# Kernel optimization log

Measured on AMD Instinct MI355X. Metric: run time of the kernel, lower is better.

Reference implementation:

```python
import jax, jax.numpy as jnp
import numpy as np

DIM = 2048
N_HEADS = 16
Q_RANK = 1536
KV_RANK = 512
D_NOPE = 128
D_ROPE = 64
D_V = 128
EPS = 1e-6
B, S = 2, 2048
ROPE_THETA = 10000.0


def rmsnorm(x, w, eps=EPS):
    return x * jax.lax.rsqrt(jnp.mean(x * x, axis=-1, keepdims=True) + eps) * w


def apply_rope(x):
    # x: [b, h, s, d] with d even; LLaMA-style interleaved pair rotation
    b, h, s, d = x.shape
    inv_freq = 1.0 / (ROPE_THETA ** (jnp.arange(0, d, 2, dtype=jnp.float32) / d))
    ang = jnp.arange(s, dtype=jnp.float32)[:, None] * inv_freq[None, :]  # [s, d/2]
    cos, sin = jnp.cos(ang), jnp.sin(ang)
    xr = x.reshape(b, h, s, d // 2, 2)
    x1, x2 = xr[..., 0], xr[..., 1]
    o1 = x1 * cos - x2 * sin
    o2 = x1 * sin + x2 * cos
    return jnp.stack([o1, o2], axis=-1).reshape(b, h, s, d)


def setup_inputs() -> dict:
    key = jax.random.key(0)
    ks = jax.random.split(key, 10)
    std = 0.02
    return {
        "x": jax.random.normal(ks[0], (B, S, DIM), dtype=jnp.float32),
        "wq_down": jax.random.normal(ks[1], (Q_RANK, DIM), dtype=jnp.float32) * std,
        "q_norm_w": jnp.ones((Q_RANK,), dtype=jnp.float32),
        "wq_up": jax.random.normal(ks[2], (N_HEADS * D_NOPE, Q_RANK), dtype=jnp.float32) * std,
        "wq_rope": jax.random.normal(ks[3], (N_HEADS * D_ROPE, Q_RANK), dtype=jnp.float32) * std,
        "wkv_down": jax.random.normal(ks[4], (KV_RANK, DIM), dtype=jnp.float32) * std,
        "kv_norm_w": jnp.ones((KV_RANK,), dtype=jnp.float32),
        "wkv_up": jax.random.normal(ks[5], (N_HEADS * (D_NOPE + D_V), KV_RANK), dtype=jnp.float32) * std,
        "wk_rope": jax.random.normal(ks[6], (D_ROPE, DIM), dtype=jnp.float32) * std,
        "wo": jax.random.normal(ks[7], (DIM, N_HEADS * D_V), dtype=jnp.float32) * std,
    }


def reference(x, wq_down, q_norm_w, wq_up, wq_rope, wkv_down, kv_norm_w, wkv_up, wk_rope, wo):
    bs, s, _ = x.shape
    # low-rank Q path
    q_c = rmsnorm(x @ wq_down.T, q_norm_w)                              # [b,s,qr]
    q_nope = (q_c @ wq_up.T).reshape(bs, s, N_HEADS, D_NOPE).transpose(0, 2, 1, 3)
    q_pe = (q_c @ wq_rope.T).reshape(bs, s, N_HEADS, D_ROPE).transpose(0, 2, 1, 3)
    # low-rank KV path
    kv_c = rmsnorm(x @ wkv_down.T, kv_norm_w)                           # [b,s,kvr]
    kv_up = (kv_c @ wkv_up.T).reshape(bs, s, N_HEADS, D_NOPE + D_V)
    k_nope = kv_up[..., :D_NOPE].transpose(0, 2, 1, 3)                  # [b,h,s,dn]
    v = kv_up[..., D_NOPE:].transpose(0, 2, 1, 3)                       # [b,h,s,dv]
    # shared rope key (1 head), broadcast across heads
    k_rope = (x @ wk_rope.T).reshape(bs, s, 1, D_ROPE).transpose(0, 2, 1, 3)  # [b,1,s,dr]
    q_pe = apply_rope(q_pe)
    k_rope = apply_rope(k_rope)
    q = jnp.concatenate([q_nope, q_pe], axis=-1)                        # [b,h,s,dn+dr]
    k = jnp.concatenate([k_nope, jnp.broadcast_to(k_rope, (bs, N_HEADS, s, D_ROPE))], axis=-1)
    scale = 1.0 / np.sqrt(D_NOPE + D_ROPE)
    scores = jnp.einsum('bhqd,bhkd->bhqk', q, k) * scale                # [b,h,s,s]
    causal = jnp.tril(jnp.ones((s, s), dtype=bool))
    scores = jnp.where(causal, scores, -jnp.inf)
    probs = jax.nn.softmax(scores, axis=-1)
    out = jnp.einsum('bhqk,bhkv->bhqv', probs, v)                       # [b,h,s,dv]
    out = out.transpose(0, 2, 1, 3).reshape(bs, s, N_HEADS * D_V)
    return out @ wo.T
```

## Files before the change

### kernel.cpp

```cpp
#include <hip/hip_runtime.h>
#include <stdint.h>

typedef _Float16 f16x8 __attribute__((ext_vector_type(8)));
typedef _Float16 f16x4 __attribute__((ext_vector_type(4)));
typedef float fx4 __attribute__((ext_vector_type(4)));

static constexpr int S_LEN = 2048;
static constexpr int BATCH = 2;
static constexpr int TOKENS = BATCH * S_LEN;
static constexpr int DIM = 2048;
static constexpr int NH = 16;
static constexpr int QR = 1536;
static constexpr int KVR = 512;
static constexpr int DN = 128;
static constexpr int DR = 64;
static constexpr int DV = 128;

__device__ __forceinline__ void async16(const _Float16* g, _Float16* lds_base_uniform) {
  __builtin_amdgcn_global_load_lds(
      (const __attribute__((address_space(1))) void*)g,
      (__attribute__((address_space(3))) void*)lds_base_uniform, 16, 0, 0);
}

__device__ __forceinline__ void bar() {
  asm volatile("" ::: "memory");
  __builtin_amdgcn_s_barrier();
  asm volatile("" ::: "memory");
}
#define VMWAIT(n) asm volatile("s_waitcnt vmcnt(" #n ")" ::: "memory")

#define ROR16(x, ctrl) \
  __uint_as_float(__builtin_amdgcn_update_dpp(__float_as_uint(x), __float_as_uint(x), \
                                              (ctrl), 0xF, 0xF, false))

__device__ __forceinline__ void sincos_rev(float ang, float* sn, float* cs) {
  float rev = ang * 0.15915494309189535f;
  rev -= floorf(rev);
  *sn = __builtin_amdgcn_sinf(rev);
  *cs = __builtin_amdgcn_cosf(rev);
}

struct CvtSegs {
  const float* src[8];
  _Float16* dst[8];
  const float* nw[8];
  int nmod[8];
  int n4[8];
  int cum[9];
};
__global__ __launch_bounds__(256) void cvt_all(CvtSegs s) {
  const int b = blockIdx.x;
  int seg = 0;
#pragma unroll
  for (int k = 0; k < 7; ++k) seg += (b >= s.cum[seg + 1]) ? 1 : 0;
  const int i = (b - s.cum[seg]) * 256 + threadIdx.x;
  if (i >= s.n4[seg]) return;
  fx4 v = *(const fx4*)(s.src[seg] + (size_t)i * 4);
  if (s.nw[seg]) {
    const int c0 = (int)(((size_t)i * 4) % (size_t)s.nmod[seg]);
    fx4 wv = *(const fx4*)(s.nw[seg] + c0);
    v[0] *= wv[0]; v[1] *= wv[1]; v[2] *= wv[2]; v[3] *= wv[3];
  }
  f16x4 o;
  o[0] = (_Float16)v[0]; o[1] = (_Float16)v[1];
  o[2] = (_Float16)v[2]; o[3] = (_Float16)v[3];
  *(f16x4*)(s.dst[seg] + (size_t)i * 4) = o;
}

__global__ __launch_bounds__(256) void rownorm(const _Float16* __restrict__ qc,
                                               const _Float16* __restrict__ kvc,
                                               float* __restrict__ rq,
                                               float* __restrict__ rkv) {
  const int idx = blockIdx.x * 4 + (threadIdx.x >> 6);
  const int lane = threadIdx.x & 63;
  const bool isq = idx < TOKENS;
  const int row = isq ? idx : idx - TOKENS;
  const int NC = isq ? QR : KVR;
  const f16x8* p = (const f16x8*)((isq ? qc : kvc) + (size_t)row * NC);
  float ss = 0.f;
  for (int c = lane; c < NC / 8; c += 64) {
    f16x8 v = p[c];
#pragma unroll
    for (int e = 0; e < 8; ++e) { const float x = (float)v[e]; ss += x * x; }
  }
#pragma unroll
  for (int d = 1; d < 64; d <<= 1) ss += __shfl_xor(ss, d);
  if (lane == 0) {
    const float rv = rsqrtf(ss / (float)NC + 1e-6f);
    if (isq) rq[row] = rv; else rkv[row] = rv;
  }
}

template <int MODE>
__global__ __launch_bounds__(256) void gemm_nt(const _Float16* __restrict__ A,
                                               const _Float16* __restrict__ W,
                                               void* __restrict__ C0v,
                                               void* __restrict__ C1v,
                                               void* __restrict__ C2v,
                                               int M, int N, int K) {
  __shared__ __attribute__((aligned(16))) _Float16 As[3][128 * 32];
  __shared__ __attribute__((aligned(16))) _Float16 Ws[3][128 * 32];
  const int tid = threadIdx.x;
  const int lane = tid & 63;
  const int wave = tid >> 6;
  const int wr = (wave >> 1) * 64;
  const int wc = (wave & 1) * 64;
  const int m16 = lane & 15;
  const int quad = lane >> 4;
  const int swz = (m16 >> 1) & 3;
  const int m0 = blockIdx.y * 128;
  const int n0 = blockIdx.x * 128;

  auto stage = [&](int buf, int k0) {
#pragma unroll
    for (int p = 0; p < 2; ++p) {
      const int cb = p * 256 + wave * 64;
      const int ch = cb + lane;
      const int r = ch >> 2;
      const int c8 = ((ch & 3) ^ ((r >> 1) & 3)) * 8;
      async16(A + (size_t)(m0 + r) * K + k0 + c8, &As[buf][cb * 8]);
      async16(W + (size_t)(n0 + r) * K + k0 + c8, &Ws[buf][cb * 8]);
    }
  };

  const fx4 fz = {0.f, 0.f, 0.f, 0.f};
  fx4 acc[4][4];
#pragma unroll
  for (int i = 0; i < 4; ++i)
#pragma unroll
    for (int j = 0; j < 4; ++j) acc[i][j] = fz;

  const int nkt = K >> 5;
  stage(0, 0);
  stage(1, 32);
  int cur = 0;
  for (int kt = 0; kt < nkt; ++kt) {
    if (kt + 1 < nkt) { VMWAIT(4); } else { VMWAIT(0); }
    bar();
    if (kt + 2 < nkt) {
      int b2 = cur + 2; if (b2 >= 3) b2 -= 3;
      stage(b2, (kt + 2) * 32);
    }
    const _Float16* as = As[cur];
    const _Float16* ws = Ws[cur];
    f16x8 af[4], wf[4];
#pragma unroll
    for (int i = 0; i < 4; ++i)
      af[i] = *(const f16x8*)(&as[((wr + i * 16 + m16) * 4 + (quad ^ swz)) * 8]);
#pragma unroll
    for (int j = 0; j < 4; ++j)
      wf[j] = *(const f16x8*)(&ws[((wc + j * 16 + m16) * 4 + (quad ^ swz)) * 8]);
#pragma unroll
    for (int i = 0; i < 4; ++i)
#pragma unroll
      for (int j = 0; j < 4; ++j)
        acc[i][j] = __builtin_amdgcn_mfma_f32_16x16x32_f16(af[i], wf[j], acc[i][j], 0, 0, 0);
    if (++cur == 3) cur = 0;
  }

#pragma unroll
  for (int j = 0; j < 4; ++j) {
    const int col = n0 + wc + j * 16 + m16;
    if (MODE == 5) {
      if (col < 2048) {
#pragma unroll
        for (int i = 0; i < 4; ++i)
#pragma unroll
          for (int r = 0; r < 4; ++r) {
            const size_t row = (size_t)(m0 + wr + i * 16 + quad * 4 + r);
            const _Float16 v = (_Float16)acc[i][j][r];
            if (col < 1536) ((_Float16*)C0v)[row * 1536 + col] = v;
            else            ((_Float16*)C1v)[row * 512 + col - 1536] = v;
          }
      } else if (col < 2112) {
        const int d = col - 2048;
        const int pidx = d >> 1;
        const bool odd = (d & 1);
        const float fr = exp2f(-(float)pidx * 0.4152410118609203f);
#pragma unroll
        for (int i = 0; i < 4; ++i)
#pragma unroll
          for (int r = 0; r < 4; ++r) {
            const size_t row = (size_t)(m0 + wr + i * 16 + quad * 4 + r);
            const int spos = (int)(row & (S_LEN - 1));
            float sn, cs;
            sincos_rev((float)spos * fr, &sn, &cs);
            const float own = acc[i][j][r];
            const float oth = __shfl_xor(own, 1);
            const float res = odd ? (oth * sn + own * cs) : (own * cs - oth * sn);
            ((_Float16*)C2v)[row * 64 + d] = (_Float16)res;
          }
      }
    } else {
      if (col < N) {
#pragma unroll
        for (int i = 0; i < 4; ++i)
#pragma unroll
          for (int r = 0; r < 4; ++r) {
            const size_t row = (size_t)(m0 + wr + i * 16 + quad * 4 + r);
            ((float*)C0v)[row * N + col] = acc[i][j][r];
          }
      }
    }
  }
}

template <int MODE>
__global__ __launch_bounds__(512, 2) void gemm256(
    const _Float16* __restrict__ Aq, const _Float16* __restrict__ Wq,
    const _Float16* __restrict__ Akv, const _Float16* __restrict__ Wkv,
    const float* __restrict__ rq, const float* __restrict__ rkv,
    void* __restrict__ C0, void* __restrict__ C1,
    void* __restrict__ C2, void* __restrict__ C3, int Kq) {
  __shared__ __attribute__((aligned(16))) _Float16 As[2][256 * 64];
  __shared__ __attribute__((aligned(16))) _Float16 Ws[2][256 * 64];

  const int tid = threadIdx.x;
  const int lane = tid & 63;
  const int wave = tid >> 6;
  const int wrow = wave >> 2;
  const int wcol = wave & 3;
  const int m16 = lane & 15;
  const int quad = lane >> 4;
  const int m0 = blockIdx.y * 256;

  const bool isq = (MODE == 0) || ((int)blockIdx.x < 12);
  const int n0 = (MODE == 0) ? blockIdx.x * 256
                             : (isq ? blockIdx.x * 256 : (blockIdx.x - 12) * 256);
  const _Float16* A = (MODE == 0) ? Aq : (isq ? Aq : Akv);
  const _Float16* W = (MODE == 0) ? Wq : (isq ? Wq : Wkv);
  const int K = (MODE == 0) ? Kq : (isq ? QR : KVR);

  auto stageHalf = [&](int buf, int k0, int tensor, int h) {
#pragma unroll
    for (int k = 0; k < 2; ++k) {
      const int cb = (wave * 2 + k) * 64;
      const int ch = cb + lane;
      const int r = ch >> 3;
      const int gc = (ch & 7) ^ (r & 7);
      const int grow = h * 128 + r;
      if (tensor == 0)
        async16(A + (size_t)(m0 + grow) * K + k0 + gc * 8,
                &As[buf][(h * 1024 + cb) * 8]);
      else
        async16(W + (size_t)(n0 + grow) * K + k0 + gc * 8,
                &Ws[buf][(h * 1024 + cb) * 8]);
    }
  };

  const fx4 fz = {0.f, 0.f, 0.f, 0.f};
  fx4 acc[8][4];
#pragma unroll
  for (int i = 0; i < 8; ++i)
#pragma unroll
    for (int j = 0; j < 4; ++j) acc[i][j] = fz;

  f16x8 af[4][2], wf0[2][2], wf1[2][2];

  auto rdA = [&](const _Float16* as, int mh) {
#pragma unroll
    for (int mg = 0; mg < 4; ++mg)
#pragma unroll
      for (int ks = 0; ks < 2; ++ks) {
        const int row = mh * 128 + mg * 32 + wrow * 16 + m16;
        af[mg][ks] = *(const f16x8*)(&as[(row * 8 + ((ks * 4 + quad) ^ (m16 & 7))) * 8]);
      }
  };
  auto rdB = [&](const _Float16* ws, int nh, f16x8 wf[2][2]) {
#pragma unroll
    for (int ng = 0; ng < 2; ++ng)
#pragma unroll
      for (int ks = 0; ks < 2; ++ks) {
        const int row = nh * 128 + ng * 64 + wcol * 16 + m16;
        wf[ng][ks] = *(const f16x8*)(&ws[(row * 8 + ((ks * 4 + quad) ^ (m16 & 7))) * 8]);
      }
  };
  auto quadMFMA = [&](int mh, int nh, f16x8 wf[2][2]) {
    __builtin_amdgcn_s_setprio(1);
#pragma unroll
    for (int ks = 0; ks < 2; ++ks)
#pragma unroll
      for (int mg = 0; mg < 4; ++mg)
#pragma unroll
        for (int ng = 0; ng < 2; ++ng)
          acc[mh * 4 + mg][nh * 2 + ng] = __builtin_amdgcn_mfma_f32_16x16x32_f16(
              af[mg][ks], wf[ng][ks], acc[mh * 4 + mg][nh * 2 + ng], 0, 0, 0);
    __builtin_amdgcn_s_setprio(0);
  };

  const int nkt = K >> 6;
  stageHalf(0, 0, 0, 0);
  stageHalf(0, 0, 1, 0);
  stageHalf(0, 0, 1, 1);
  stageHalf(0, 0, 0, 1);

  for (int t = 0; t < nkt; ++t) {
    const int cur = t & 1;
    const int nb = cur ^ 1;
    const int k0n = (t + 1) * 64;
    const bool more = (t + 1 < nkt);
    const _Float16* as = As[cur];
    const _Float16* ws = Ws[cur];

    VMWAIT(4);
    bar();
    rdA(as, 0);
    rdB(ws, 0, wf0);
    if (more) stageHalf(nb, k0n, 0, 0);
    quadMFMA(0, 0, wf0);

    if (more) { VMWAIT(4); } else { VMWAIT(2); }
    bar();
    rdB(ws, 1, wf1);
    if (more) stageHalf(nb, k0n, 1, 0);
    quadMFMA(0, 1, wf1);

    if (more) { VMWAIT(4); } else { VMWAIT(0); }
    bar();
    rdA(as, 1);
    if (more) stageHalf(nb, k0n, 1, 1);
    quadMFMA(1, 1, wf1);

    bar();
    if (more) stageHalf(nb, k0n, 0, 1);
    quadMFMA(1, 0, wf0);
  }

  float rsq[8][4];
  if (MODE == 1) {
    const float* rs = isq ? rq : rkv;
#pragma unroll
    for (int mg = 0; mg < 8; ++mg)
#pragma unroll
      for (int r = 0; r < 4; ++r)
        rsq[mg][r] = rs[m0 + mg * 32 + wrow * 16 + quad * 4 + r];
  }

#pragma unroll
  for (int ng = 0; ng < 4; ++ng) {
    const int col = n0 + ng * 64 + wcol * 16 + m16;
    if (MODE == 0) {
#pragma unroll
      for (int mg = 0; mg < 8; ++mg)
#pragma unroll
        for (int r = 0; r < 4; ++r) {
          const size_t row = (size_t)(m0 + mg * 32 + wrow * 16 + quad * 4 + r);
          ((float*)C0)[row * 2048 + col] = acc[mg][ng][r];
        }
    } else if (isq) {
#pragma unroll
      for (int mg = 0; mg < 8; ++mg)
#pragma unroll
        for (int r = 0; r < 4; ++r) {
          const size_t row = (size_t)(m0 + mg * 32 + wrow * 16 + quad * 4 + r);
          const _Float16 v = (_Float16)(acc[mg][ng][r] * rsq[mg][r]);
          if (col < 2048) ((_Float16*)C0)[row * 2048 + col] = v;
          else ((_Float16*)C1)[row * 1024 + col - 2048] = v;
        }
    } else {
      const int head = col >> 8;
      const int sub = col & 255;
      if (sub < 128) {
#pragma unroll
        for (int mg = 0; mg < 8; ++mg)
#pragma unroll
          for (int r = 0; r < 4; ++r) {
            const size_t row = (size_t)(m0 + mg * 32 + wrow * 16 + quad * 4 + r);
            ((_Float16*)C2)[row * 2048 + head * 128 + sub] =
                (_Float16)(acc[mg][ng][r] * rsq[mg][r]);
          }
      } else {
        const int dv = sub - 128;
#pragma unroll
        for (int mg = 0; mg < 8; ++mg) {
          f16x4 v;
#pragma unroll
          for (int r = 0; r < 4; ++r) v[r] = (_Float16)(acc[mg][ng][r] * rsq[mg][r]);
          *(f16x4*)(&((_Float16*)C3)[(size_t)(head * 128 + dv) * TOKENS + m0 +
                                     mg * 32 + wrow * 16 + quad * 4]) = v;
        }
      }
    }
  }
}

__global__ __launch_bounds__(512, 1) void gemm_out(
    const _Float16* __restrict__ A,
    const _Float16* __restrict__ W,
    float* __restrict__ C) {
  __shared__ __attribute__((aligned(16))) _Float16 As[2][128 * 64];
  __shared__ __attribute__((aligned(16))) _Float16 Ws[2][256 * 64];

  const int tid = threadIdx.x;
  const int lane = tid & 63;
  const int wave = tid >> 6;
  const int wrow = wave >> 2;
  const int wcol = wave & 3;
  const int m16 = lane & 15;
  const int quad = lane >> 4;
  const int m0 = blockIdx.y * 128;
  const int n0 = blockIdx.x * 256;
  const int K = NH * DV;

  auto stageA = [&](int buf, int k0) {
#pragma unroll
    for (int k = 0; k < 2; ++k) {
      const int cb = (wave * 2 + k) * 64;
      const int ch = cb + lane;
      const int r = ch >> 3;
      const int gc = (ch & 7) ^ (r & 7);
      async16(A + (size_t)(m0 + r) * K + k0 + gc * 8, &As[buf][cb * 8]);
    }
  };
  auto stageW = [&](int buf, int k0, int h) {
#pragma unroll
    for (int k = 0; k < 2; ++k) {
      const int cb = (wave * 2 + k) * 64;
      const int ch = cb + lane;
      const int r = ch >> 3;
      const int gc = (ch & 7) ^ (r & 7);
      async16(W + (size_t)(n0 + h * 128 + r) * K + k0 + gc * 8,
              &Ws[buf][(h * 1024 + cb) * 8]);
    }
  };

  const fx4 fz = {0.f, 0.f, 0.f, 0.f};
  fx4 acc[4][4];
#pragma unroll
  for (int i = 0; i < 4; ++i)
#pragma unroll
    for (int j = 0; j < 4; ++j) acc[i][j] = fz;

  f16x8 af[4][2], wf0[2][2], wf1[2][2];

  auto rdA = [&](const _Float16* as) {
#pragma unroll
    for (int mg = 0; mg < 4; ++mg)
#pragma unroll
      for (int ks = 0; ks < 2; ++ks) {
        const int row = mg * 32 + wrow * 16 + m16;
        af[mg][ks] = *(const f16x8*)(&as[(row * 8 + ((ks * 4 + quad) ^ (m16 & 7))) * 8]);
      }
  };
  auto rdB = [&](const _Float16* ws, int nh, f16x8 wf[2][2]) {
#pragma unroll
    for (int ng = 0; ng < 2; ++ng)
#pragma unroll
      for (int ks = 0; ks < 2; ++ks) {
        const int row = nh * 128 + ng * 64 + wcol * 16 + m16;
        wf[ng][ks] = *(const f16x8*)(&ws[(row * 8 + ((ks * 4 + quad) ^ (m16 & 7))) * 8]);
      }
  };
  auto halfMFMA = [&](int nh, f16x8 wf[2][2]) {
    __builtin_amdgcn_s_setprio(1);
#pragma unroll
    for (int ks = 0; ks < 2; ++ks)
#pragma unroll
      for (int mg = 0; mg < 4; ++mg)
#pragma unroll
        for (int ng = 0; ng < 2; ++ng)
          acc[mg][nh * 2 + ng] = __builtin_amdgcn_mfma_f32_16x16x32_f16(
              af[mg][ks], wf[ng][ks], acc[mg][nh * 2 + ng], 0, 0, 0);
    __builtin_amdgcn_s_setprio(0);
  };

  const int nkt = K >> 6;
  stageA(0, 0);
  stageW(0, 0, 0);
  stageW(0, 0, 1);

  for (int t = 0; t < nkt; ++t) {
    const int cur = t & 1;
    const int nb = cur ^ 1;
    const int k0n = (t + 1) * 64;
    const bool more = (t + 1 < nkt);
    const _Float16* as = As[cur];
    const _Float16* ws = Ws[cur];

    VMWAIT(2);
    bar();
    rdA(as);
    rdB(ws, 0, wf0);
    if (more) stageA(nb, k0n);
    halfMFMA(0, wf0);

    if (more) { VMWAIT(2); } else { VMWAIT(0); }
    bar();
    rdB(ws, 1, wf1);
    if (more) { stageW(nb, k0n, 0); stageW(nb, k0n, 1); }
    halfMFMA(1, wf1);
  }

#pragma unroll
  for (int ng = 0; ng < 4; ++ng) {
    const int col = n0 + ng * 64 + wcol * 16 + m16;
#pragma unroll
    for (int mg = 0; mg < 4; ++mg)
#pragma unroll
      for (int r = 0; r < 4; ++r) {
        const size_t row = (size_t)(m0 + mg * 32 + wrow * 16 + quad * 4 + r);
        C[row * 2048 + col] = acc[mg][ng][r];
      }
  }
}

__global__ __launch_bounds__(512, 2) void mla_attn(
    const _Float16* __restrict__ qn,
    const _Float16* __restrict__ qp,
    const _Float16* __restrict__ kn,
    const _Float16* __restrict__ kr,
    const _Float16* __restrict__ vT,
    _Float16* __restrict__ out)
{
  __shared__ __attribute__((aligned(16))) _Float16 Ks[2][768 * 8];
  __shared__ __attribute__((aligned(16))) _Float16 Vs[2][512 * 8];
  __shared__ __attribute__((aligned(16))) _Float16 Ps[8][16][40];

  const int bid = blockIdx.x;
  const int j = bid >> 5;
  const int bh = bid & 31;
  const int b = bh >> 4;
  const int h = bh & 15;
  const int q16 = 15 - j;
  const int qb = q16 * 128;
  const int tok0 = b * S_LEN;

  const int tid = threadIdx.x;
  const int lane = tid & 63;
  const int wave = tid >> 6;
  const int m16 = lane & 15;
  const int quad = lane >> 4;
  const int R0 = qb + wave * 16;

  auto stageKV = [&](int buf, int kbase) {
#pragma unroll
    for (int jj = 0; jj < 3; ++jj) {
      const int idx = wave * 3 + jj;
      if (idx < 12) {
        const int ch = idx * 2 + (lane >> 5);
        const int key = lane & 31;
        const _Float16* g = (ch < 16)
            ? kn + (size_t)(tok0 + kbase + key) * 2048 + h * 128 + ch * 8
            : kr + (size_t)(tok0 + kbase + key) * 64 + (ch - 16) * 8;
        async16(g, &Ks[buf][idx * 512]);
      } else if (idx < 20) {
        const int iv = idx - 12;
        const int p = iv * 64 + lane;
        const int L = p ^ ((p >> 3) & 3);
        const int dv = L >> 2;
        const int qcc = L & 3;
        async16(vT + (size_t)(h * 128 + dv) * TOKENS + tok0 + kbase + qcc * 8,
                &Vs[buf][iv * 512]);
      }
    }
  };

  const float scale2 = 0.07216878364870323f * 1.4426950408889634f;
  const fx4 fz = {0.f, 0.f, 0.f, 0.f};

  f16x8 qf[6];
  {
    const int srow = qb + wave * 16 + m16;
    const size_t t = (size_t)(tok0 + srow);
#pragma unroll
    for (int kk = 0; kk < 4; ++kk)
      qf[kk] = *(const f16x8*)(qn + t * 2048 + h * 128 + kk * 32 + quad * 8);
#pragma unroll
    for (int kk = 0; kk < 2; ++kk) {
      f16x8 v = *(const f16x8*)(qp + t * 1024 + h * 64 + kk * 32 + quad * 8);
      f16x8 o;
      const int i0 = kk * 16 + quad * 4;
#pragma unroll
      for (int jj = 0; jj < 4; ++jj) {
        const float ang = (float)srow * exp2f(-(float)(i0 + jj) * 0.4152410118609203f);
        float sn, cs;
        sincos_rev(ang, &sn, &cs);
        const float x1 = (float)v[2 * jj], x2 = (float)v[2 * jj + 1];
        o[2 * jj]     = (_Float16)(x1 * cs - x2 * sn);
        o[2 * jj + 1] = (_Float16)(x1 * sn + x2 * cs);
      }
      qf[4 + kk] = o;
    }
  }

  fx4 oacc[9];
#pragma unroll
  for (int n = 0; n < 9; ++n) oacc[n] = fz;
  float mst[4];
#pragma unroll
  for (int r = 0; r < 4; ++r) mst[r] = -3.0e38f;
  f16x8 vones;
#pragma unroll
  for (int e = 0; e < 8; ++e) vones[e] = (_Float16)1.0f;

  const int nkt = (qb >> 5) + 4;

  stageKV(0, 0);
  for (int kt = 0; kt < nkt; ++kt) {
    const int kbase = kt * 32;
    __syncthreads();
    if (kt + 1 < nkt) stageKV((kt + 1) & 1, kbase + 32);

    const bool live = (kbase <= R0 + 15);
    if (!live) continue;
    const _Float16* ks = Ks[kt & 1];
    const _Float16* vs = Vs[kt & 1];

    fx4 sc[2];
    sc[0] = fz; sc[1] = fz;
    __builtin_amdgcn_s_setprio(1);
#pragma unroll
    for (int kk = 0; kk < 6; ++kk) {
#pragma unroll
      for (int n = 0; n < 2; ++n) {
        f16x8 kf = *(const f16x8*)(&ks[(kk * 128 + quad * 32 + n * 16 + m16) * 8]);
        sc[n] = __builtin_amdgcn_mfma_f32_16x16x32_f16(qf[kk], kf, sc[n], 0, 0, 0);
      }
    }
    __builtin_amdgcn_s_setprio(0);

    f16x8 vf[8];
#pragma unroll
    for (int n8 = 0; n8 < 8; ++n8) {
      const int c0 = (n8 * 16 + m16) * 4 + quad;
      vf[n8] = *(const f16x8*)(&vs[(c0 ^ ((c0 >> 3) & 3)) * 8]);
    }

    const bool needmask = (kbase + 31 > R0);
    float alpha[4];
    bool any_upd = false;
#pragma unroll
    for (int r = 0; r < 4; ++r) {
      float v0 = sc[0][r] * scale2;
      float v1 = sc[1][r] * scale2;
      if (needmask) {
        const int qrow = R0 + quad * 4 + r;
        if (kbase + m16 > qrow)      v0 = -3.0e38f;
        if (kbase + 16 + m16 > qrow) v1 = -3.0e38f;
      }
      const float pre = fmaxf(v0, v1);
      float al = 1.0f;
      if (__any(pre > mst[r] + 10.0f)) {
        float mx = pre;
        mx = fmaxf(mx, ROR16(mx, 0x128));
        mx = fmaxf(mx, ROR16(mx, 0x124));
        mx = fmaxf(mx, ROR16(mx, 0x122));
        mx = fmaxf(mx, ROR16(mx, 0x121));
        const float mn = fmaxf(mst[r], mx);
        al = exp2f(mst[r] - mn);
        mst[r] = mn;
        any_upd = true;
      }
      alpha[r] = al;
      const float p0 = exp2f(v0 - mst[r]);
      const float p1 = exp2f(v1 - mst[r]);
      _Float16* pr = &Ps[wave][quad * 4 + r][0];
      pr[m16] = (_Float16)p0;
      pr[16 + m16] = (_Float16)p1;
    }
    if (any_upd) {
#pragma unroll
      for (int n8 = 0; n8 < 9; ++n8)
#pragma unroll
        for (int r = 0; r < 4; ++r) oacc[n8][r] *= alpha[r];
    }

    f16x8 pf = *(const f16x8*)(&Ps[wave][m16][quad * 8]);
    __builtin_amdgcn_s_setprio(1);
#pragma unroll
    for (int n8 = 0; n8 < 8; ++n8)
      oacc[n8] = __builtin_amdgcn_mfma_f32_16x16x32_f16(pf, vf[n8], oacc[n8], 0, 0, 0);
    oacc[8] = __builtin_amdgcn_mfma_f32_16x16x32_f16(pf, vones, oacc[8], 0, 0, 0);
    __builtin_amdgcn_s_setprio(0);
  }

  float inv[4];
#pragma unroll
  for (int r = 0; r < 4; ++r) inv[r] = 1.0f / oacc[8][r];
#pragma unroll
  for (int n8 = 0; n8 < 8; ++n8) {
#pragma unroll
    for (int r = 0; r < 4; ++r) {
      const size_t t = (size_t)(tok0 + qb + wave * 16 + quad * 4 + r);
      out[t * 2048 + h * 128 + n8 * 16 + m16] = (_Float16)(oacc[n8][r] * inv[r]);
    }
  }
}

extern "C" void kernel_launch(void* const* d_in, const int* in_sizes, int n_in,
                              void* d_out, int out_size, void* d_ws, size_t ws_size,
                              hipStream_t stream) {
  const float* x         = (const float*)d_in[0];
  const float* wq_down   = (const float*)d_in[1];
  const float* q_norm_w  = (const float*)d_in[2];
  const float* wq_up     = (const float*)d_in[3];
  const float* wq_rope   = (const float*)d_in[4];
  const float* wkv_down  = (const float*)d_in[5];
  const float* kv_norm_w = (const float*)d_in[6];
  const float* wkv_up    = (const float*)d_in[7];
  const float* wk_rope   = (const float*)d_in[8];
  const float* wo        = (const float*)d_in[9];
  float* out = (float*)d_out;

  char* ws = (char*)d_ws;
  size_t off = 0;
  auto alloc = [&](size_t bytes) {
    char* p = ws + off;
    off += (bytes + 255) & ~(size_t)255;
    return p;
  };
  _Float16* x_h     = (_Float16*)alloc((size_t)TOKENS * DIM * 2);
  _Float16* wA_h    = (_Float16*)alloc((size_t)2176 * DIM * 2);
  _Float16* wquqr_h = (_Float16*)alloc((size_t)3072 * QR * 2);
  _Float16* wkvu_h  = (_Float16*)alloc((size_t)NH * 256 * KVR * 2);
  _Float16* wo_h    = (_Float16*)alloc((size_t)DIM * NH * DV * 2);
  _Float16* qc_h    = (_Float16*)alloc((size_t)TOKENS * QR * 2);
  _Float16* kvc_h   = (_Float16*)alloc((size_t)TOKENS * KVR * 2);
  _Float16* qnope_h = (_Float16*)alloc((size_t)TOKENS * 2048 * 2);
  _Float16* qpe_h   = (_Float16*)alloc((size_t)TOKENS * 1024 * 2);
  _Float16* knope_h = (_Float16*)alloc((size_t)TOKENS * 2048 * 2);
  _Float16* vT_h    = (_Float16*)alloc((size_t)2048 * TOKENS * 2);
  _Float16* krope_h = (_Float16*)alloc((size_t)TOKENS * DR * 2);
  _Float16* attn_h  = (_Float16*)alloc((size_t)TOKENS * 2048 * 2);
  float* rq_h       = (float*)alloc((size_t)TOKENS * 4);
  float* rkv_h      = (float*)alloc((size_t)TOKENS * 4);

  CvtSegs cs;
  const float* srcs[8] = {x, wq_down, wq_up, wq_rope, wkv_down, wk_rope, wkv_up, wo};
  _Float16* dsts[8] = {x_h, wA_h, wquqr_h, wquqr_h + (size_t)2048 * QR,
                       wA_h + (size_t)1536 * DIM, wA_h + (size_t)2048 * DIM,
                       wkvu_h, wo_h};
  const float* nws[8] = {nullptr, nullptr, q_norm_w, q_norm_w, nullptr, nullptr,
                         kv_norm_w, nullptr};
  const int nmods[8] = {4, 4, QR, QR, 4, 4, KVR, 4};
  const size_t ns[8] = {(size_t)TOKENS * DIM, (size_t)QR * DIM, (size_t)2048 * QR,
                        (size_t)1024 * QR, (size_t)KVR * DIM, (size_t)DR * DIM,
                        (size_t)NH * 256 * KVR, (size_t)DIM * NH * DV};
  int cum = 0;
  for (int i = 0; i < 8; ++i) {
    cs.src[i] = srcs[i];
    cs.dst[i] = dsts[i];
    cs.nw[i] = nws[i];
    cs.nmod[i] = nmods[i];
    cs.n4[i] = (int)(ns[i] / 4);
    cs.cum[i] = cum;
    cum += (cs.n4[i] + 255) / 256;
  }
  cs.cum[8] = cum;
  cvt_all<<<dim3(cum), 256, 0, stream>>>(cs);

  const unsigned gm = TOKENS / 128;

  gemm_nt<5><<<dim3(17, gm), 256, 0, stream>>>(x_h, wA_h, qc_h, kvc_h, krope_h,
                                               TOKENS, 2112, DIM);
  rownorm<<<dim3(2 * TOKENS / 4), 256, 0, stream>>>(qc_h, kvc_h, rq_h, rkv_h);
  gemm256<1><<<dim3(12 + 16, TOKENS / 256), 512, 0, stream>>>(
      qc_h, wquqr_h, kvc_h, wkvu_h, rq_h, rkv_h,
      qnope_h, qpe_h, knope_h, vT_h, 0);
  mla_attn<<<dim3(512), 512, 0, stream>>>(qnope_h, qpe_h, knope_h, krope_h, vT_h, attn_h);
  gemm_out<<<dim3(8, 32), 512, 0, stream>>>(attn_h, wo_h, out);
}
```

Baseline: 440.3 us.

## Fuse RMSNorm statistics into a larger-tile down-projection GEMM epilogue

Replaces the 128x128 down-projection GEMM with a 512-thread 128x256-tile kernel that uses a double-buffered 64-wide K loop. Its epilogue also accumulates per-row sums of squares into global buffers with atomics. This removes the separate rownorm kernel and the re-read of qc/kvc it needed; the up-projection now computes rsqrt from those sums. The sum buffers are zeroed by an extra segment in the conversion kernel. Risks are a 288-block grid that slightly exceeds one wave of CUs, and padded weight rows that are computed but then discarded.

```diff
diff --git a/kernel.cpp b/kernel.cpp
--- a/kernel.cpp
+++ b/kernel.cpp
@@ -41,20 +41,27 @@
 }
 
 struct CvtSegs {
-  const float* src[8];
-  _Float16* dst[8];
-  const float* nw[8];
-  int nmod[8];
-  int n4[8];
-  int cum[9];
+  const float* src[9];
+  _Float16* dst[9];
+  const float* nw[9];
+  int nmod[9];
+  int n4[9];
+  int cum[10];
 };
 __global__ __launch_bounds__(256) void cvt_all(CvtSegs s) {
   const int b = blockIdx.x;
   int seg = 0;
 #pragma unroll
-  for (int k = 0; k < 7; ++k) seg += (b >= s.cum[seg + 1]) ? 1 : 0;
+  for (int k = 0; k < 8; ++k) seg += (b >= s.cum[seg + 1]) ? 1 : 0;
   const int i = (b - s.cum[seg]) * 256 + threadIdx.x;
   if (i >= s.n4[seg]) return;
+  if (!s.src[seg]) {
+    f16x4 z;
+    z[0] = (_Float16)0.f; z[1] = (_Float16)0.f;
+    z[2] = (_Float16)0.f; z[3] = (_Float16)0.f;
+    *(f16x4*)(s.dst[seg] + (size_t)i * 4) = z;
+    return;
+  }
   fx4 v = *(const fx4*)(s.src[seg] + (size_t)i * 4);
   if (s.nw[seg]) {
     const int c0 = (int)(((size_t)i * 4) % (size_t)s.nmod[seg]);
@@ -67,59 +74,45 @@
   *(f16x4*)(s.dst[seg] + (size_t)i * 4) = o;
 }
 
-__global__ __launch_bounds__(256) void rownorm(const _Float16* __restrict__ qc,
-                                               const _Float16* __restrict__ kvc,
-                                               float* __restrict__ rq,
-                                               float* __restrict__ rkv) {
-  const int idx = blockIdx.x * 4 + (threadIdx.x >> 6);
-  const int lane = threadIdx.x & 63;
-  const bool isq = idx < TOKENS;
-  const int row = isq ? idx : idx - TOKENS;
-  const int NC = isq ? QR : KVR;
-  const f16x8* p = (const f16x8*)((isq ? qc : kvc) + (size_t)row * NC);
-  float ss = 0.f;
-  for (int c = lane; c < NC / 8; c += 64) {
-    f16x8 v = p[c];
-#pragma unroll
-    for (int e = 0; e < 8; ++e) { const float x = (float)v[e]; ss += x * x; }
-  }
-#pragma unroll
-  for (int d = 1; d < 64; d <<= 1) ss += __shfl_xor(ss, d);
-  if (lane == 0) {
-    const float rv = rsqrtf(ss / (float)NC + 1e-6f);
-    if (isq) rq[row] = rv; else rkv[row] = rv;
-  }
-}
-
-template <int MODE>
-__global__ __launch_bounds__(256) void gemm_nt(const _Float16* __restrict__ A,
-                                               const _Float16* __restrict__ W,
-                                               void* __restrict__ C0v,
-                                               void* __restrict__ C1v,
-                                               void* __restrict__ C2v,
-                                               int M, int N, int K) {
-  __shared__ __attribute__((aligned(16))) _Float16 As[3][128 * 32];
-  __shared__ __attribute__((aligned(16))) _Float16 Ws[3][128 * 32];
+__global__ __launch_bounds__(512, 1) void gemm_down(
+    const _Float16* __restrict__ A,
+    const _Float16* __restrict__ W,
+    _Float16* __restrict__ qc, _Float16* __restrict__ kvc,
+    _Float16* __restrict__ kr,
+    float* __restrict__ sums_q, float* __restrict__ sums_kv) {
+  __shared__ __attribute__((aligned(16))) _Float16 As[2][128 * 64];
+  __shared__ __attribute__((aligned(16))) _Float16 Ws[2][256 * 64];
+
   const int tid = threadIdx.x;
   const int lane = tid & 63;
   const int wave = tid >> 6;
-  const int wr = (wave >> 1) * 64;
-  const int wc = (wave & 1) * 64;
+  const int wrow = wave >> 2;
+  const int wcol = wave & 3;
   const int m16 = lane & 15;
   const int quad = lane >> 4;
-  const int swz = (m16 >> 1) & 3;
   const int m0 = blockIdx.y * 128;
-  const int n0 = blockIdx.x * 128;
-
-  auto stage = [&](int buf, int k0) {
-#pragma unroll
-    for (int p = 0; p < 2; ++p) {
-      const int cb = p * 256 + wave * 64;
+  const int n0 = blockIdx.x * 256;
+  const int K = DIM;
+
+  auto stageA = [&](int buf, int k0) {
+#pragma unroll
+    for (int k = 0; k < 2; ++k) {
+      const int cb = (wave * 2 + k) * 64;
       const int ch = cb + lane;
-      const int r = ch >> 2;
-      const int c8 = ((ch & 3) ^ ((r >> 1) & 3)) * 8;
-      async16(A + (size_t)(m0 + r) * K + k0 + c8, &As[buf][cb * 8]);
-      async16(W + (size_t)(n0 + r) * K + k0 + c8, &Ws[buf][cb * 8]);
+      const int r = ch >> 3;
+      const int gc = (ch & 7) ^ (r & 7);
+      async16(A + (size_t)(m0 + r) * K + k0 + gc * 8, &As[buf][cb * 8]);
+    }
+  };
+  auto stageW = [&](int buf, int k0, int h) {
+#pragma unroll
+    for (int k = 0; k < 2; ++k) {
+      const int cb = (wave * 2 + k) * 64;
+      const int ch = cb + lane;
+      const int r = ch >> 3;
+      const int gc = (ch & 7) ^ (r & 7);
+      async16(W + (size_t)(n0 + h * 128 + r) * K + k0 + gc * 8,
+              &Ws[buf][(h * 1024 + cb) * 8]);
     }
   };
 
@@ -130,88 +123,134 @@
 #pragma unroll
     for (int j = 0; j < 4; ++j) acc[i][j] = fz;
 
-  const int nkt = K >> 5;
-  stage(0, 0);
-  stage(1, 32);
-  int cur = 0;
-  for (int kt = 0; kt < nkt; ++kt) {
-    if (kt + 1 < nkt) { VMWAIT(4); } else { VMWAIT(0); }
-    bar();
-    if (kt + 2 < nkt) {
-      int b2 = cur + 2; if (b2 >= 3) b2 -= 3;
-      stage(b2, (kt + 2) * 32);
-    }
+  f16x8 af[4][2], wf0[2][2], wf1[2][2];
+
+  auto rdA = [&](const _Float16* as) {
+#pragma unroll
+    for (int mg = 0; mg < 4; ++mg)
+#pragma unroll
+      for (int ks = 0; ks < 2; ++ks) {
+        const int row = mg * 32 + wrow * 16 + m16;
+        af[mg][ks] = *(const f16x8*)(&as[(row * 8 + ((ks * 4 + quad) ^ (m16 & 7))) * 8]);
+      }
+  };
+  auto rdB = [&](const _Float16* ws, int nh, f16x8 wf[2][2]) {
+#pragma unroll
+    for (int ng = 0; ng < 2; ++ng)
+#pragma unroll
+      for (int ks = 0; ks < 2; ++ks) {
+        const int row = nh * 128 + ng * 64 + wcol * 16 + m16;
+        wf[ng][ks] = *(const f16x8*)(&ws[(row * 8 + ((ks * 4 + quad) ^ (m16 & 7))) * 8]);
+      }
+  };
+  auto halfMFMA = [&](int nh, f16x8 wf[2][2]) {
+    __builtin_amdgcn_s_setprio(1);
+#pragma unroll
+    for (int ks = 0; ks < 2; ++ks)
+#pragma unroll
+      for (int mg = 0; mg < 4; ++mg)
+#pragma unroll
+        for (int ng = 0; ng < 2; ++ng)
+          acc[mg][nh * 2 + ng] = __builtin_amdgcn_mfma_f32_16x16x32_f16(
+              af[mg][ks], wf[ng][ks], acc[mg][nh * 2 + ng], 0, 0, 0);
+    __builtin_amdgcn_s_setprio(0);
+  };
+
+  const int nkt = K >> 6;
+  stageA(0, 0);
+  stageW(0, 0, 0);
+  stageW(0, 0, 1);
+
+  for (int t = 0; t < nkt; ++t) {
+    const int cur = t & 1;
+    const int nb = cur ^ 1;
+    const int k0n = (t + 1) * 64;
+    const bool more = (t + 1 < nkt);
     const _Float16* as = As[cur];
     const _Float16* ws = Ws[cur];
-    f16x8 af[4], wf[4];
-#pragma unroll
-    for (int i = 0; i < 4; ++i)
-      af[i] = *(const f16x8*)(&as[((wr + i * 16 + m16) * 4 + (quad ^ swz)) * 8]);
-#pragma unroll
-    for (int j = 0; j < 4; ++j)
-      wf[j] = *(const f16x8*)(&ws[((wc + j * 16 + m16) * 4 + (quad ^ swz)) * 8]);
-#pragma unroll
-    for (int i = 0; i < 4; ++i)
-#pragma unroll
-      for (int j = 0; j < 4; ++j)
-        acc[i][j] = __builtin_amdgcn_mfma_f32_16x16x32_f16(af[i], wf[j], acc[i][j], 0, 0, 0);
-    if (++cur == 3) cur = 0;
-  }
-
-#pragma unroll
-  for (int j = 0; j < 4; ++j) {
-    const int col = n0 + wc + j * 16 + m16;
-    if (MODE == 5) {
-      if (col < 2048) {
-#pragma unroll
-        for (int i = 0; i < 4; ++i)
-#pragma unroll
-          for (int r = 0; r < 4; ++r) {
-            const size_t row = (size_t)(m0 + wr + i * 16 + quad * 4 + r);
-            const _Float16 v = (_Float16)acc[i][j][r];
-            if (col < 1536) ((_Float16*)C0v)[row * 1536 + col] = v;
-            else            ((_Float16*)C1v)[row * 512 + col - 1536] = v;
-          }
-      } else if (col < 2112) {
+
+    VMWAIT(2);
+    bar();
+    rdA(as);
+    rdB(ws, 0, wf0);
+    if (more) stageA(nb, k0n);
+    halfMFMA(0, wf0);
+
+    if (more) { VMWAIT(2); } else { VMWAIT(0); }
+    bar();
+    rdB(ws, 1, wf1);
+    if (more) { stageW(nb, k0n, 0); stageW(nb, k0n, 1); }
+    halfMFMA(1, wf1);
+  }
+
+  const int bx = blockIdx.x;
+  if (bx < 8) {
+#pragma unroll
+    for (int ng = 0; ng < 4; ++ng) {
+      const int col = n0 + ng * 64 + wcol * 16 + m16;
+#pragma unroll
+      for (int mg = 0; mg < 4; ++mg)
+#pragma unroll
+        for (int r = 0; r < 4; ++r) {
+          const size_t row = (size_t)(m0 + mg * 32 + wrow * 16 + quad * 4 + r);
+          const _Float16 v = (_Float16)acc[mg][ng][r];
+          if (bx < 6) qc[row * 1536 + col] = v;
+          else        kvc[row * 512 + col - 1536] = v;
+        }
+    }
+    float* sums = (bx < 6) ? sums_q : sums_kv;
+#pragma unroll
+    for (int mg = 0; mg < 4; ++mg)
+#pragma unroll
+      for (int r = 0; r < 4; ++r) {
+        float p = 0.f;
+#pragma unroll
+        for (int ng = 0; ng < 4; ++ng) p += acc[mg][ng][r] * acc[mg][ng][r];
+        p += __shfl_xor(p, 1);
+        p += __shfl_xor(p, 2);
+        p += __shfl_xor(p, 4);
+        p += __shfl_xor(p, 8);
+        if (m16 == 0)
+          atomicAdd(&sums[m0 + mg * 32 + wrow * 16 + quad * 4 + r], p);
+      }
+  } else {
+#pragma unroll
+    for (int ng = 0; ng < 4; ++ng) {
+      const int col = n0 + ng * 64 + wcol * 16 + m16;
+      if (col < 2112) {
         const int d = col - 2048;
         const int pidx = d >> 1;
         const bool odd = (d & 1);
         const float fr = exp2f(-(float)pidx * 0.4152410118609203f);
 #pragma unroll
-        for (int i = 0; i < 4; ++i)
+        for (int mg = 0; mg < 4; ++mg)
 #pragma unroll
           for (int r = 0; r < 4; ++r) {
-            const size_t row = (size_t)(m0 + wr + i * 16 + quad * 4 + r);
+            const size_t row = (size_t)(m0 + mg * 32 + wrow * 16 + quad * 4 + r);
             const int spos = (int)(row & (S_LEN - 1));
             float sn, cs;
             sincos_rev((float)spos * fr, &sn, &cs);
-            const float own = acc[i][j][r];
+            const float own = acc[mg][ng][r];
             const float oth = __shfl_xor(own, 1);
             const float res = odd ? (oth * sn + own * cs) : (own * cs - oth * sn);
-            ((_Float16*)C2v)[row * 64 + d] = (_Float16)res;
+            kr[row * 64 + d] = (_Float16)res;
           }
-      }
-    } else {
-      if (col < N) {
-#pragma unroll
-        for (int i = 0; i < 4; ++i)
-#pragma unroll
-          for (int r = 0; r < 4; ++r) {
-            const size_t row = (size_t)(m0 + wr + i * 16 + quad * 4 + r);
-            ((float*)C0v)[row * N + col] = acc[i][j][r];
-          }
-      }
-    }
-  }
-}
-
-template <int MODE>
-__global__ __launch_bounds__(512, 2) void gemm256(
-    const _Float16* __restrict__ Aq, const _Float16* __restrict__ Wq,
-    const _Float16* __restrict__ Akv, const _Float16* __restrict__ Wkv,
-    const float* __restrict__ rq, const float* __restrict__ rkv,
-    void* __restrict__ C0, void* __restrict__ C1,
-    void* __restrict__ C2, void* __restrict__ C3, int Kq) {
+      } else {
+#pragma unroll
+        for (int mg = 0; mg < 4; ++mg)
+#pragma unroll
+          for (int r = 0; r < 4; ++r) (void)__shfl_xor(acc[mg][ng][r], 1);
+      }
+    }
+  }
+}
+
+__global__ __launch_bounds__(512, 2) void gemm256_up(
+    const _Float16* __restrict__ qc, const _Float16* __restrict__ wqu,
+    const _Float16* __restrict__ kvc, const _Float16* __restrict__ wkvu,
+    const float* __restrict__ sums_q, const float* __restrict__ sums_kv,
+    _Float16* __restrict__ qnope, _Float16* __restrict__ qpe,
+    _Float16* __restrict__ knope, _Float16* __restrict__ vT) {
   __shared__ __attribute__((aligned(16))) _Float16 As[2][256 * 64];
   __shared__ __attribute__((aligned(16))) _Float16 Ws[2][256 * 64];
 
@@ -224,12 +263,11 @@
   const int quad = lane >> 4;
   const int m0 = blockIdx.y * 256;
 
-  const bool isq = (MODE == 0) || ((int)blockIdx.x < 12);
-  const int n0 = (MODE == 0) ? blockIdx.x * 256
-                             : (isq ? blockIdx.x * 256 : (blockIdx.x - 12) * 256);
-  const _Float16* A = (MODE == 0) ? Aq : (isq ? Aq : Akv);
-  const _Float16* W = (MODE == 0) ? Wq : (isq ? Wq : Wkv);
-  const int K = (MODE == 0) ? Kq : (isq ? QR : KVR);
+  const bool isq = ((int)blockIdx.x < 12);
+  const int n0 = (isq ? blockIdx.x : blockIdx.x - 12) * 256;
+  const _Float16* A = isq ? qc : kvc;
+  const _Float16* W = isq ? wqu : wkvu;
+  const int K = isq ? QR : KVR;
 
   auto stageHalf = [&](int buf, int k0, int tensor, int h) {
 #pragma unroll
@@ -326,36 +364,27 @@
     quadMFMA(1, 0, wf0);
   }
 
+  const float* rs = isq ? sums_q : sums_kv;
+  const float invNC = isq ? (1.0f / (float)QR) : (1.0f / (float)KVR);
   float rsq[8][4];
-  if (MODE == 1) {
-    const float* rs = isq ? rq : rkv;
-#pragma unroll
-    for (int mg = 0; mg < 8; ++mg)
-#pragma unroll
-      for (int r = 0; r < 4; ++r)
-        rsq[mg][r] = rs[m0 + mg * 32 + wrow * 16 + quad * 4 + r];
-  }
+#pragma unroll
+  for (int mg = 0; mg < 8; ++mg)
+#pragma unroll
+    for (int r = 0; r < 4; ++r)
+      rsq[mg][r] = rsqrtf(rs[m0 + mg * 32 + wrow * 16 + quad * 4 + r] * invNC + 1e-6f);
 
 #pragma unroll
   for (int ng = 0; ng < 4; ++ng) {
     const int col = n0 + ng * 64 + wcol * 16 + m16;
-    if (MODE == 0) {
-#pragma unroll
-      for (int mg = 0; mg < 8; ++mg)
-#pragma unroll
-        for (int r = 0; r < 4; ++r) {
-          const size_t row = (size_t)(m0 + mg * 32 + wrow * 16 + quad * 4 + r);
-          ((float*)C0)[row * 2048 + col] = acc[mg][ng][r];
-        }
-    } else if (isq) {
+    if (isq) {
 #pragma unroll
       for (int mg = 0; mg < 8; ++mg)
 #pragma unroll
         for (int r = 0; r < 4; ++r) {
           const size_t row = (size_t)(m0 + mg * 32 + wrow * 16 + quad * 4 + r);
           const _Float16 v = (_Float16)(acc[mg][ng][r] * rsq[mg][r]);
-          if (col < 2048) ((_Float16*)C0)[row * 2048 + col] = v;
-          else ((_Float16*)C1)[row * 1024 + col - 2048] = v;
+          if (col < 2048) qnope[row * 2048 + col] = v;
+          else qpe[row * 1024 + col - 2048] = v;
         }
     } else {
       const int head = col >> 8;
@@ -366,7 +395,7 @@
 #pragma unroll
           for (int r = 0; r < 4; ++r) {
             const size_t row = (size_t)(m0 + mg * 32 + wrow * 16 + quad * 4 + r);
-            ((_Float16*)C2)[row * 2048 + head * 128 + sub] =
+            knope[row * 2048 + head * 128 + sub] =
                 (_Float16)(acc[mg][ng][r] * rsq[mg][r]);
           }
       } else {
@@ -376,8 +405,8 @@
           f16x4 v;
 #pragma unroll
           for (int r = 0; r < 4; ++r) v[r] = (_Float16)(acc[mg][ng][r] * rsq[mg][r]);
-          *(f16x4*)(&((_Float16*)C3)[(size_t)(head * 128 + dv) * TOKENS + m0 +
-                                     mg * 32 + wrow * 16 + quad * 4]) = v;
+          *(f16x4*)(&vT[(size_t)(head * 128 + dv) * TOKENS + m0 +
+                        mg * 32 + wrow * 16 + quad * 4]) = v;
         }
       }
     }
@@ -710,7 +739,7 @@
     return p;
   };
   _Float16* x_h     = (_Float16*)alloc((size_t)TOKENS * DIM * 2);
-  _Float16* wA_h    = (_Float16*)alloc((size_t)2176 * DIM * 2);
+  _Float16* wA_h    = (_Float16*)alloc((size_t)2304 * DIM * 2);
   _Float16* wquqr_h = (_Float16*)alloc((size_t)3072 * QR * 2);
   _Float16* wkvu_h  = (_Float16*)alloc((size_t)NH * 256 * KVR * 2);
   _Float16* wo_h    = (_Float16*)alloc((size_t)DIM * NH * DV * 2);
@@ -722,22 +751,24 @@
   _Float16* vT_h    = (_Float16*)alloc((size_t)2048 * TOKENS * 2);
   _Float16* krope_h = (_Float16*)alloc((size_t)TOKENS * DR * 2);
   _Float16* attn_h  = (_Float16*)alloc((size_t)TOKENS * 2048 * 2);
-  float* rq_h       = (float*)alloc((size_t)TOKENS * 4);
-  float* rkv_h      = (float*)alloc((size_t)TOKENS * 4);
+  float* sq_h       = (float*)alloc((size_t)TOKENS * 4);
+  float* skv_h      = (float*)alloc((size_t)TOKENS * 4);
 
   CvtSegs cs;
-  const float* srcs[8] = {x, wq_down, wq_up, wq_rope, wkv_down, wk_rope, wkv_up, wo};
-  _Float16* dsts[8] = {x_h, wA_h, wquqr_h, wquqr_h + (size_t)2048 * QR,
+  const float* srcs[9] = {x, wq_down, wq_up, wq_rope, wkv_down, wk_rope, wkv_up, wo,
+                          nullptr};
+  _Float16* dsts[9] = {x_h, wA_h, wquqr_h, wquqr_h + (size_t)2048 * QR,
                        wA_h + (size_t)1536 * DIM, wA_h + (size_t)2048 * DIM,
-                       wkvu_h, wo_h};
-  const float* nws[8] = {nullptr, nullptr, q_norm_w, q_norm_w, nullptr, nullptr,
-                         kv_norm_w, nullptr};
-  const int nmods[8] = {4, 4, QR, QR, 4, 4, KVR, 4};
-  const size_t ns[8] = {(size_t)TOKENS * DIM, (size_t)QR * DIM, (size_t)2048 * QR,
+                       wkvu_h, wo_h, (_Float16*)sq_h};
+  const float* nws[9] = {nullptr, nullptr, q_norm_w, q_norm_w, nullptr, nullptr,
+                         kv_norm_w, nullptr, nullptr};
+  const int nmods[9] = {4, 4, QR, QR, 4, 4, KVR, 4, 4};
+  const size_t ns[9] = {(size_t)TOKENS * DIM, (size_t)QR * DIM, (size_t)2048 * QR,
                         (size_t)1024 * QR, (size_t)KVR * DIM, (size_t)DR * DIM,
-                        (size_t)NH * 256 * KVR, (size_t)DIM * NH * DV};
+                        (size_t)NH * 256 * KVR, (size_t)DIM * NH * DV,
+                        (size_t)2 * TOKENS * 2};
   int cum = 0;
-  for (int i = 0; i < 8; ++i) {
+  for (int i = 0; i < 9; ++i) {
     cs.src[i] = srcs[i];
     cs.dst[i] = dsts[i];
     cs.nw[i] = nws[i];
@@ -746,17 +777,14 @@
     cs.cum[i] = cum;
     cum += (cs.n4[i] + 255) / 256;
   }
-  cs.cum[8] = cum;
+  cs.cum[9] = cum;
   cvt_all<<<dim3(cum), 256, 0, stream>>>(cs);
 
-  const unsigned gm = TOKENS / 128;
-
-  gemm_nt<5><<<dim3(17, gm), 256, 0, stream>>>(x_h, wA_h, qc_h, kvc_h, krope_h,
-                                               TOKENS, 2112, DIM);
-  rownorm<<<dim3(2 * TOKENS / 4), 256, 0, stream>>>(qc_h, kvc_h, rq_h, rkv_h);
-  gemm256<1><<<dim3(12 + 16, TOKENS / 256), 512, 0, stream>>>(
-      qc_h, wquqr_h, kvc_h, wkvu_h, rq_h, rkv_h,
-      qnope_h, qpe_h, knope_h, vT_h, 0);
+  gemm_down<<<dim3(9, 32), 512, 0, stream>>>(x_h, wA_h, qc_h, kvc_h, krope_h,
+                                             sq_h, skv_h);
+  gemm256_up<<<dim3(12 + 16, TOKENS / 256), 512, 0, stream>>>(
+      qc_h, wquqr_h, kvc_h, wkvu_h, sq_h, skv_h,
+      qnope_h, qpe_h, knope_h, vT_h);
   mla_attn<<<dim3(512), 512, 0, stream>>>(qnope_h, qpe_h, knope_h, krope_h, vT_h, attn_h);
   gemm_out<<<dim3(8, 32), 512, 0, stream>>>(attn_h, wo_h, out);
 }
```

After: 454.8 us. 3.3% more time.
